# Kernel tuning notes

Measured on AMD Instinct MI355X. Metric: run time of the kernel, lower is better.

Reference implementation:

```python
import jax, jax.numpy as jnp
import numpy as np

B, D, E, N = 2048, 4096, 512, 8192
BN_EPS = 1e-5
COS_EPS = 1e-8


def setup_inputs() -> dict:
    key = jax.random.key(0)
    k1, k2, k3, k4, k5 = jax.random.split(key, 5)
    vf = jax.random.normal(k1, (B, D), dtype=jnp.float32)
    p_wfs = jax.random.normal(k2, (B, D), dtype=jnp.float32)
    n_wfs = jax.random.normal(k3, (N, E), dtype=jnp.float32)
    # BatchNorm1d(4096) affine params (default init gamma=1, beta=0; use random-ish gamma for generality)
    gamma = jnp.ones((D,), dtype=jnp.float32)
    beta = jnp.zeros((D,), dtype=jnp.float32)
    # Linear(D -> E)
    lim = 1.0 / np.sqrt(D)
    W = jax.random.uniform(k4, (E, D), dtype=jnp.float32, minval=-lim, maxval=lim)
    b = jax.random.uniform(k5, (E,), dtype=jnp.float32, minval=-lim, maxval=lim)
    return {"vf": vf, "p_wfs": p_wfs, "n_wfs": n_wfs, "gamma": gamma, "beta": beta, "W": W, "b": b}


def _row_normalize(x, eps=COS_EPS):
    nrm = jnp.sqrt(jnp.sum(x * x, axis=-1, keepdims=True))
    return x / jnp.maximum(nrm, eps)


def reference(vf, p_wfs, n_wfs, gamma, beta, W, b):
    # BatchNorm1d in training mode: batch mean / biased variance over the batch dim
    mean = jnp.mean(vf, axis=0)
    var = jnp.mean((vf - mean) ** 2, axis=0)
    vfn = (vf - mean) * (gamma / jnp.sqrt(var + BN_EPS)) + beta  # [B, D]

    # Linear + ReLU embedding
    emb = jax.nn.relu(vfn @ W.T + b)  # [B, E]

    # p_e: row-wise cosine(normed vf, p_wfs) -> [B]
    p_e = jnp.sum(_row_normalize(vfn) * _row_normalize(p_wfs), axis=-1)

    # n_e: cosine(emb[v], n_wfs[n]) for all v,n -> one normalized GEMM [B, N]
    n_e = _row_normalize(emb) @ _row_normalize(n_wfs).T

    n_neg = n_wfs.shape[0]
    n_e_stack = n_e.reshape(-1, 1)                      # [B*N, 1]
    p_e_stack = jnp.repeat(p_e, n_neg).reshape(-1, 1)   # [B*N, 1], p_e[v] repeated N times
    return (n_e_stack, p_e_stack)
```

## Files before the change

### kernel.cpp

```cpp
#include <hip/hip_runtime.h>
#include <stdint.h>
#include <stddef.h>

#define B_ 2048
#define D_ 4096
#define E_ 512
#define N_ 8192
#define SPLITK 4

typedef unsigned short ushort_t;
typedef __attribute__((ext_vector_type(8))) short short8;
typedef __attribute__((ext_vector_type(4))) float floatx4;
typedef __attribute__((ext_vector_type(4))) unsigned short ushort4_t;

__device__ __forceinline__ void async_load16(const void* g, void* l) {
  __builtin_amdgcn_global_load_lds((__attribute__((address_space(1))) void*)(g),
                                   (__attribute__((address_space(3))) void*)(l), 16, 0, 0);
}

__device__ __forceinline__ ushort_t f2bf(float f) {
  unsigned int u = __float_as_uint(f);
  unsigned int r = (u + 0x7fffu + ((u >> 16) & 1u)) >> 16;
  return (ushort_t)r;
}
__device__ __forceinline__ float bf2f(ushort_t h) {
  return __uint_as_float(((unsigned int)h) << 16);
}

__global__ __launch_bounds__(256) void bn_partial(const float* __restrict__ vf,
                                                  float* __restrict__ psum,
                                                  float* __restrict__ psq) {
  int d4 = blockIdx.x * 256 + threadIdx.x;
  int chunk = blockIdx.y;
  floatx4 s = {0.f, 0.f, 0.f, 0.f}, q = {0.f, 0.f, 0.f, 0.f};
  int r0 = chunk * 32;
  for (int r = r0; r < r0 + 32; ++r) {
    floatx4 v = ((const floatx4*)(vf + (size_t)r * D_))[d4];
    s += v; q += v * v;
  }
  ((floatx4*)(psum + (size_t)chunk * D_))[d4] = s;
  ((floatx4*)(psq  + (size_t)chunk * D_))[d4] = q;
}

__global__ __launch_bounds__(256) void prep_all(const float* __restrict__ psum,
                                                const float* __restrict__ psq,
                                                const float* __restrict__ gamma,
                                                const float* __restrict__ beta,
                                                const float* __restrict__ W,
                                                const float* __restrict__ nw,
                                                float* __restrict__ scale,
                                                float* __restrict__ shift,
                                                ushort_t* __restrict__ wb,
                                                ushort_t* __restrict__ nwb,
                                                float* __restrict__ inv_nw) {
  int bid = blockIdx.x;
  if (bid < 4) {
    int d4 = bid * 256 + threadIdx.x;
    floatx4 s = {0.f, 0.f, 0.f, 0.f}, q = {0.f, 0.f, 0.f, 0.f};
    for (int c = 0; c < 64; ++c) {
      s += ((const floatx4*)(psum + (size_t)c * D_))[d4];
      q += ((const floatx4*)(psq  + (size_t)c * D_))[d4];
    }
    floatx4 g = ((const floatx4*)gamma)[d4];
    floatx4 bt = ((const floatx4*)beta)[d4];
    floatx4 sc, sh;
#pragma unroll
    for (int j = 0; j < 4; ++j) {
      float mean = s[j] * (1.0f / B_);
      float var  = q[j] * (1.0f / B_) - mean * mean;
      float scj  = g[j] * rsqrtf(var + 1e-5f);
      sc[j] = scj;
      sh[j] = bt[j] - mean * scj;
    }
    ((floatx4*)scale)[d4] = sc;
    ((floatx4*)shift)[d4] = sh;
  } else if (bid < 2052) {
    size_t i = ((size_t)(bid - 4) * 256 + threadIdx.x) * 4;
    floatx4 x = *(const floatx4*)(W + i);
    ushort4_t o;
#pragma unroll
    for (int j = 0; j < 4; ++j) o[j] = f2bf(x[j]);
    *(ushort4_t*)(wb + i) = o;
  } else {
    int wv = threadIdx.x >> 6, l = threadIdx.x & 63;
    int n = (bid - 2052) * 4 + wv;
    const floatx4* src = (const floatx4*)(nw + (size_t)n * E_);
    ushort4_t* dst = (ushort4_t*)(nwb + (size_t)n * E_);
    float s = 0.f;
#pragma unroll
    for (int k = 0; k < 2; ++k) {
      floatx4 x = src[l + 64 * k];
      ushort4_t o;
#pragma unroll
      for (int j = 0; j < 4; ++j) { o[j] = f2bf(x[j]); s += x[j] * x[j]; }
      dst[l + 64 * k] = o;
    }
    for (int off = 32; off; off >>= 1) s += __shfl_down(s, off);
    if (l == 0) inv_nw[n] = 1.f / fmaxf(sqrtf(s), 1e-8f);
  }
}

__global__ __launch_bounds__(256) void pe_cast(const float* __restrict__ vf,
                                               const float* __restrict__ p,
                                               const float* __restrict__ scale,
                                               const float* __restrict__ shift,
                                               ushort_t* __restrict__ vfn,
                                               float* __restrict__ pe) {
  int wv = threadIdx.x >> 6, l = threadIdx.x & 63;
  int v = blockIdx.x * 4 + wv;
  const floatx4* vf4 = (const floatx4*)(vf + (size_t)v * D_);
  const floatx4* p4  = (const floatx4*)(p  + (size_t)v * D_);
  const floatx4* sc4 = (const floatx4*)scale;
  const floatx4* sh4 = (const floatx4*)shift;
  ushort_t* vrow = vfn + (size_t)v * D_;
  float sd = 0.f, sa = 0.f, sb = 0.f;
#pragma unroll 4
  for (int k = 0; k < 16; ++k) {
    int i = l + 64 * k;
    floatx4 x = vf4[i], y = p4[i], s = sc4[i], t = sh4[i];
    ushort4_t o;
#pragma unroll
    for (int j = 0; j < 4; ++j) {
      float xn = x[j] * s[j] + t[j];
      o[j] = f2bf(xn);
      sd += xn * y[j]; sa += xn * xn; sb += y[j] * y[j];
    }
    *(ushort4_t*)(vrow + i * 4) = o;
  }
  for (int off = 32; off; off >>= 1) {
    sd += __shfl_down(sd, off); sa += __shfl_down(sa, off); sb += __shfl_down(sb, off);
  }
  if (l == 0) {
    float na = fmaxf(sqrtf(sa), 1e-8f), nb = fmaxf(sqrtf(sb), 1e-8f);
    pe[v] = sd / (na * nb);
  }
}

template <int BM, int BN, int BK, int WCOLS, int MT, int NT>
__device__ __forceinline__ void gemm_core(const ushort_t* __restrict__ A,
                                          const ushort_t* __restrict__ Bt, int K,
                                          int kb, int ke, int bm0, int bn0,
                                          ushort_t* As, ushort_t* Bs,
                                          floatx4 (&acc)[MT][NT]) {
  const int tid = threadIdx.x, w = tid >> 6, l = tid & 63;
  constexpr int ISS_A = BM * BK / 2048;
  constexpr int ISS_B = BN * BK / 2048;
  const int wr = w / WCOLS, wc = w % WCOLS;
  const int m16 = l & 15, q = l >> 4;

  for (int k0 = kb; k0 < ke; k0 += BK) {
#pragma unroll
    for (int i = 0; i < ISS_A; ++i) {
      int e = i * 2048 + tid * 8;
      int row = e / BK, col = e % BK;
      async_load16(A + (size_t)(bm0 + row) * K + (k0 + col), &As[i * 2048 + w * 512]);
    }
#pragma unroll
    for (int i = 0; i < ISS_B; ++i) {
      int e = i * 2048 + tid * 8;
      int row = e / BK, col = e % BK;
      async_load16(Bt + (size_t)(bn0 + row) * K + (k0 + col), &Bs[i * 2048 + w * 512]);
    }
    __syncthreads();
#pragma unroll
    for (int kc = 0; kc < BK / 32; ++kc) {
      short8 af[MT], bf[NT];
#pragma unroll
      for (int i = 0; i < MT; ++i)
        af[i] = *(const short8*)&As[(wr * (MT * 16) + i * 16 + m16) * BK + kc * 32 + q * 8];
#pragma unroll
      for (int j = 0; j < NT; ++j)
        bf[j] = *(const short8*)&Bs[(wc * (NT * 16) + j * 16 + m16) * BK + kc * 32 + q * 8];
#pragma unroll
      for (int i = 0; i < MT; ++i)
#pragma unroll
        for (int j = 0; j < NT; ++j)
          acc[i][j] = __builtin_amdgcn_mfma_f32_16x16x32_bf16(af[i], bf[j], acc[i][j], 0, 0, 0);
    }
    __syncthreads();
  }
}

__global__ __launch_bounds__(256, 2) void gemm1_splitk(const ushort_t* __restrict__ A,
                                                       const ushort_t* __restrict__ Bt,
                                                       float* __restrict__ partial) {
  __shared__ __align__(16) ushort_t As[128 * 64];
  __shared__ __align__(16) ushort_t Bs[64 * 64];
  floatx4 acc[4][2] = {};
  int bm0 = blockIdx.y * 128, bn0 = blockIdx.x * 64, s = blockIdx.z;
  int kb = s * (D_ / SPLITK);
  gemm_core<128, 64, 64, 2, 4, 2>(A, Bt, D_, kb, kb + D_ / SPLITK, bm0, bn0, As, Bs, acc);
  int tid = threadIdx.x, w = tid >> 6, l = tid & 63, m16 = l & 15, q = l >> 4;
  int wr = w >> 1, wc = w & 1;
  float* out = partial + (size_t)s * B_ * E_;
#pragma unroll
  for (int i = 0; i < 4; ++i)
#pragma unroll
    for (int j = 0; j < 2; ++j) {
      int col = bn0 + wc * 32 + j * 16 + m16;
#pragma unroll
      for (int r = 0; r < 4; ++r) {
        int row = bm0 + wr * 64 + i * 16 + q * 4 + r;
        out[(size_t)row * E_ + col] = acc[i][j][r];
      }
    }
}

__global__ __launch_bounds__(256) void gemm1_reduce(const float* __restrict__ partial,
                                                    const float* __restrict__ bias,
                                                    ushort_t* __restrict__ emb,
                                                    float* __restrict__ inv_emb) {
  int wv = threadIdx.x >> 6, l = threadIdx.x & 63;
  int row = blockIdx.x * 4 + wv;
  float sumsq = 0.f;
#pragma unroll
  for (int k = 0; k < 2; ++k) {
    int i = l + 64 * k;
    floatx4 v = {0.f, 0.f, 0.f, 0.f};
#pragma unroll
    for (int s = 0; s < SPLITK; ++s)
      v += ((const floatx4*)(partial + (size_t)s * B_ * E_ + (size_t)row * E_))[i];
    floatx4 bb = ((const floatx4*)bias)[i];
    ushort4_t o;
#pragma unroll
    for (int j = 0; j < 4; ++j) {
      float f = fmaxf(v[j] + bb[j], 0.f);
      o[j] = f2bf(f);
      float fb = bf2f(o[j]);
      sumsq += fb * fb;
    }
    ((ushort4_t*)(emb + (size_t)row * E_))[i] = o;
  }
  for (int off = 32; off; off >>= 1) sumsq += __shfl_down(sumsq, off);
  if (l == 0) inv_emb[row] = 1.f / fmaxf(sqrtf(sumsq), 1e-8f);
}

#define BAR() asm volatile("s_barrier" ::: "memory")
#define VMW(n) asm volatile("s_waitcnt vmcnt(" #n ")" ::: "memory")

__device__ __forceinline__ void stage_A2(const ushort_t* __restrict__ A, ushort_t* Abuf,
                                         int bm0, int tk, int h, int tid) {
#pragma unroll
  for (int j = 0; j < 2; ++j) {
    int off = j * 8192 + tid * 16;
    int sl = off >> 7;
    int cb = off & 127;
    int r  = ((sl >> 6) & 1) * 128 + h * 64 + (sl & 63);
    int cg = cb ^ ((sl & 7) << 4);
    async_load16(A + (size_t)(bm0 + r) * E_ + tk * 64 + (cg >> 1),
                 Abuf + h * 8192 + j * 4096 + (tid >> 6) * 512);
  }
}

__device__ __forceinline__ void stage_B2(const ushort_t* __restrict__ Bt, ushort_t* Bbuf,
                                         int bn0, int tk, int h, int tid) {
#pragma unroll
  for (int j = 0; j < 2; ++j) {
    int off = j * 8192 + tid * 16;
    int sl = off >> 7;
    int cb = off & 127;
    int r  = ((sl >> 5) & 3) * 64 + h * 32 + (sl & 31);
    int cg = cb ^ ((sl & 7) << 4);
    async_load16(Bt + (size_t)(bn0 + r) * E_ + tk * 64 + (cg >> 1),
                 Bbuf + h * 8192 + j * 4096 + (tid >> 6) * 512);
  }
}

template <int MH, int NH>
__device__ __forceinline__ void ph_loads(const ushort_t* Ab, const ushort_t* Bb,
                                         int wr, int wc, int m16, int co0, int co1,
                                         short8 (&af)[4][2], short8 (&bfr)[2][2]) {
#pragma unroll
  for (int f = 0; f < 4; ++f) {
    const ushort_t* p = Ab + (MH * 128 + wr * 64 + f * 16 + m16) * 64;
    af[f][0] = *(const short8*)(p + co0);
    af[f][1] = *(const short8*)(p + co1);
  }
#pragma unroll
  for (int g = 0; g < 2; ++g) {
    const ushort_t* p = Bb + (NH * 128 + wc * 32 + g * 16 + m16) * 64;
    bfr[g][0] = *(const short8*)(p + co0);
    bfr[g][1] = *(const short8*)(p + co1);
  }
}

template <int MH, int NH>
__device__ __forceinline__ void ph_mma(const short8 (&af)[4][2], const short8 (&bfr)[2][2],
                                       floatx4 (&acc)[2][2][4][2]) {
  __builtin_amdgcn_s_setprio(1);
#pragma unroll
  for (int kc = 0; kc < 2; ++kc)
#pragma unroll
    for (int f = 0; f < 4; ++f)
#pragma unroll
      for (int g = 0; g < 2; ++g)
        acc[MH][NH][f][g] =
            __builtin_amdgcn_mfma_f32_16x16x32_bf16(af[f][kc], bfr[g][kc], acc[MH][NH][f][g], 0, 0, 0);
  __builtin_amdgcn_s_setprio(0);
}

__device__ __forceinline__ void out2_batch(float* __restrict__ out2, float pew,
                                           int bm0, int bn0, int b, int w, int l) {
#pragma unroll
  for (int rr = 0; rr < 4; ++rr) {
    float v = __uint_as_float(__builtin_amdgcn_readlane(__float_as_uint(pew), b * 4 + rr));
    int row = bm0 + w * 32 + b * 4 + rr;
    floatx4 vv = {v, v, v, v};
    *(floatx4*)(out2 + (size_t)row * N_ + bn0 + (l << 2)) = vv;
  }
}

#define PH(MH, NH, AB, BB, STAGE, WAIT) \
  { short8 af[4][2]; short8 bfr[2][2];                                  \
    ph_loads<MH, NH>(AB, BB, wr, wc, m16, co0, co1, af, bfr);           \
    STAGE; WAIT;                                                        \
    BAR();                                                              \
    ph_mma<MH, NH>(af, bfr, acc);                                       \
    BAR(); }

__global__ __launch_bounds__(512, 2) void gemm2_8ph(const ushort_t* __restrict__ A,
                                                    const ushort_t* __restrict__ Bt,
                                                    const float* __restrict__ inv_a,
                                                    const float* __restrict__ inv_b,
                                                    const float* __restrict__ pe,
                                                    float* __restrict__ out) {
  __shared__ __align__(16) ushort_t As_[2][16384];
  __shared__ __align__(16) ushort_t Bs_[2][16384];
  const int tid = threadIdx.x, w = tid >> 6, l = tid & 63;
  const int m16 = l & 15, q = l >> 4;
  const int wr = w >> 2, wc = w & 3;
  const int bm0 = blockIdx.y * 256, bn0 = blockIdx.x * 256;
  const int swz = (m16 & 7) << 4;
  const int co0 = ((q * 16) ^ swz) >> 1;
  const int co1 = ((64 + q * 16) ^ swz) >> 1;
  float* out2 = out + (size_t)B_ * N_;

  floatx4 acc[2][2][4][2] = {};

  float pew = pe[bm0 + w * 32 + (l & 31)];
  VMW(0);

  stage_A2(A, As_[0], bm0, 0, 0, tid);
  stage_A2(A, As_[0], bm0, 0, 1, tid);
  stage_B2(Bt, Bs_[0], bn0, 0, 0, tid);
  stage_B2(Bt, Bs_[0], bn0, 0, 1, tid);
  stage_A2(A, As_[1], bm0, 1, 0, tid);
  stage_B2(Bt, Bs_[1], bn0, 1, 0, tid);
  VMW(4);
  BAR();

#pragma unroll
  for (int i = 0; i < 4; ++i) {
    const int t1 = 2 * i + 1, t2 = 2 * i + 2, t3 = 2 * i + 3;
    const bool pre = (i < 3);
    out2_batch(out2, pew, bm0, bn0, 2 * i, w, l);
    PH(0, 0, As_[0], Bs_[0], stage_A2(A, As_[1], bm0, t1, 1, tid), ;)
    PH(0, 1, As_[0], Bs_[0], stage_B2(Bt, Bs_[1], bn0, t1, 1, tid), ;)
    PH(1, 0, As_[0], Bs_[0], if (pre) stage_A2(A, As_[0], bm0, t2, 0, tid), ;)
    PH(1, 1, As_[0], Bs_[0],
       if (pre) stage_B2(Bt, Bs_[0], bn0, t2, 0, tid),
       if (pre) { VMW(4); } else { VMW(0); })
    out2_batch(out2, pew, bm0, bn0, 2 * i + 1, w, l);
    PH(0, 0, As_[1], Bs_[1], if (pre) stage_A2(A, As_[0], bm0, t2, 1, tid), ;)
    PH(0, 1, As_[1], Bs_[1], if (pre) stage_B2(Bt, Bs_[0], bn0, t2, 1, tid), ;)
    PH(1, 0, As_[1], Bs_[1], if (pre) stage_A2(A, As_[1], bm0, t3, 0, tid), ;)
    PH(1, 1, As_[1], Bs_[1],
       if (pre) stage_B2(Bt, Bs_[1], bn0, t3, 0, tid),
       if (pre) { VMW(4); })
  }

  float ibv[2][2];
#pragma unroll
  for (int nh = 0; nh < 2; ++nh)
#pragma unroll
    for (int g = 0; g < 2; ++g)
      ibv[nh][g] = inv_b[bn0 + wc * 64 + nh * 32 + g * 16 + m16];
#pragma unroll
  for (int mh = 0; mh < 2; ++mh)
#pragma unroll
    for (int f = 0; f < 4; ++f)
#pragma unroll
      for (int rr = 0; rr < 4; ++rr) {
        int row = bm0 + wr * 128 + mh * 64 + f * 16 + q * 4 + rr;
        float ia = inv_a[row];
        size_t base = (size_t)row * N_ + bn0 + wc * 64;
#pragma unroll
        for (int nh = 0; nh < 2; ++nh)
#pragma unroll
          for (int g = 0; g < 2; ++g)
            out[base + nh * 32 + g * 16 + m16] = acc[mh][nh][f][g][rr] * ia * ibv[nh][g];
      }
}

extern "C" void kernel_launch(void* const* d_in, const int* in_sizes, int n_in,
                              void* d_out, int out_size, void* d_ws, size_t ws_size,
                              hipStream_t stream) {
  (void)in_sizes; (void)n_in; (void)out_size; (void)ws_size;
  const float* vf    = (const float*)d_in[0];
  const float* p_wfs = (const float*)d_in[1];
  const float* n_wfs = (const float*)d_in[2];
  const float* gamma = (const float*)d_in[3];
  const float* beta  = (const float*)d_in[4];
  const float* W     = (const float*)d_in[5];
  const float* bias  = (const float*)d_in[6];
  float* out = (float*)d_out;

  char* ws = (char*)d_ws;
  float* psum    = (float*)ws;  ws += (size_t)64 * D_ * 4;
  float* psq     = (float*)ws;  ws += (size_t)64 * D_ * 4;
  float* scale   = (float*)ws;  ws += (size_t)D_ * 4;
  float* shift   = (float*)ws;  ws += (size_t)D_ * 4;
  float* pe      = (float*)ws;  ws += (size_t)B_ * 4;
  float* inv_nw  = (float*)ws;  ws += (size_t)N_ * 4;
  float* inv_emb = (float*)ws;  ws += (size_t)B_ * 4;
  float* partial = (float*)ws;  ws += (size_t)SPLITK * B_ * E_ * 4;
  ushort_t* vfn  = (ushort_t*)ws;  ws += (size_t)B_ * D_ * 2;
  ushort_t* wb   = (ushort_t*)ws;  ws += (size_t)E_ * D_ * 2;
  ushort_t* nwb  = (ushort_t*)ws;  ws += (size_t)N_ * E_ * 2;
  ushort_t* emb  = (ushort_t*)ws;  ws += (size_t)B_ * E_ * 2;

  bn_partial<<<dim3(D_ / 1024, 64), 256, 0, stream>>>(vf, psum, psq);
  prep_all<<<4 + 2048 + N_ / 4, 256, 0, stream>>>(psum, psq, gamma, beta, W, n_wfs,
                                                  scale, shift, wb, nwb, inv_nw);
  pe_cast<<<B_ / 4, 256, 0, stream>>>(vf, p_wfs, scale, shift, vfn, pe);
  gemm1_splitk<<<dim3(E_ / 64, B_ / 128, SPLITK), 256, 0, stream>>>(vfn, wb, partial);
  gemm1_reduce<<<B_ / 4, 256, 0, stream>>>(partial, bias, emb, inv_emb);
  gemm2_8ph<<<dim3(N_ / 256, B_ / 256), 512, 0, stream>>>(emb, nwb, inv_emb, inv_nw, pe, out);
}
```

Before: 271.7 us.

## Double-buffer split-K GEMM1 with swizzled LDS and async prefetch pipeline

Replaces the generic single-buffered gemm_core in the first split-K GEMM with a dedicated two-stage pipeline. Global-to-LDS loads for tile t+2 are issued while MFMAs run on the current tile, with explicit vmcnt/lgkmcnt waits and raw barriers. An XOR swizzle on LDS columns is added to cut bank conflicts, along with s_setprio around the MFMA block. The cost is double the LDS per block, which may reduce occupancy, and more delicate hand-written wait and barrier ordering.

```diff
diff --git a/kernel.cpp b/kernel.cpp
--- a/kernel.cpp
+++ b/kernel.cpp
@@ -26,6 +26,10 @@
 __device__ __forceinline__ float bf2f(ushort_t h) {
   return __uint_as_float(((unsigned int)h) << 16);
 }
+
+#define BAR() asm volatile("s_barrier" ::: "memory")
+#define VMW(n) asm volatile("s_waitcnt vmcnt(" #n ")" ::: "memory")
+#define LGKM0() asm volatile("s_waitcnt lgkmcnt(0)" ::: "memory")
 
 __global__ __launch_bounds__(256) void bn_partial(const float* __restrict__ vf,
                                                   float* __restrict__ psum,
@@ -136,63 +140,80 @@
   }
 }
 
-template <int BM, int BN, int BK, int WCOLS, int MT, int NT>
-__device__ __forceinline__ void gemm_core(const ushort_t* __restrict__ A,
-                                          const ushort_t* __restrict__ Bt, int K,
-                                          int kb, int ke, int bm0, int bn0,
-                                          ushort_t* As, ushort_t* Bs,
-                                          floatx4 (&acc)[MT][NT]) {
-  const int tid = threadIdx.x, w = tid >> 6, l = tid & 63;
-  constexpr int ISS_A = BM * BK / 2048;
-  constexpr int ISS_B = BN * BK / 2048;
-  const int wr = w / WCOLS, wc = w % WCOLS;
-  const int m16 = l & 15, q = l >> 4;
-
-  for (int k0 = kb; k0 < ke; k0 += BK) {
-#pragma unroll
-    for (int i = 0; i < ISS_A; ++i) {
-      int e = i * 2048 + tid * 8;
-      int row = e / BK, col = e % BK;
-      async_load16(A + (size_t)(bm0 + row) * K + (k0 + col), &As[i * 2048 + w * 512]);
-    }
-#pragma unroll
-    for (int i = 0; i < ISS_B; ++i) {
-      int e = i * 2048 + tid * 8;
-      int row = e / BK, col = e % BK;
-      async_load16(Bt + (size_t)(bn0 + row) * K + (k0 + col), &Bs[i * 2048 + w * 512]);
-    }
-    __syncthreads();
-#pragma unroll
-    for (int kc = 0; kc < BK / 32; ++kc) {
-      short8 af[MT], bf[NT];
-#pragma unroll
-      for (int i = 0; i < MT; ++i)
-        af[i] = *(const short8*)&As[(wr * (MT * 16) + i * 16 + m16) * BK + kc * 32 + q * 8];
-#pragma unroll
-      for (int j = 0; j < NT; ++j)
-        bf[j] = *(const short8*)&Bs[(wc * (NT * 16) + j * 16 + m16) * BK + kc * 32 + q * 8];
-#pragma unroll
-      for (int i = 0; i < MT; ++i)
-#pragma unroll
-        for (int j = 0; j < NT; ++j)
-          acc[i][j] = __builtin_amdgcn_mfma_f32_16x16x32_bf16(af[i], bf[j], acc[i][j], 0, 0, 0);
-    }
-    __syncthreads();
-  }
-}
-
 __global__ __launch_bounds__(256, 2) void gemm1_splitk(const ushort_t* __restrict__ A,
                                                        const ushort_t* __restrict__ Bt,
                                                        float* __restrict__ partial) {
-  __shared__ __align__(16) ushort_t As[128 * 64];
-  __shared__ __align__(16) ushort_t Bs[64 * 64];
+  __shared__ __align__(16) ushort_t As[2][128 * 64];
+  __shared__ __align__(16) ushort_t Bs[2][64 * 64];
   floatx4 acc[4][2] = {};
-  int bm0 = blockIdx.y * 128, bn0 = blockIdx.x * 64, s = blockIdx.z;
-  int kb = s * (D_ / SPLITK);
-  gemm_core<128, 64, 64, 2, 4, 2>(A, Bt, D_, kb, kb + D_ / SPLITK, bm0, bn0, As, Bs, acc);
-  int tid = threadIdx.x, w = tid >> 6, l = tid & 63, m16 = l & 15, q = l >> 4;
-  int wr = w >> 1, wc = w & 1;
-  float* out = partial + (size_t)s * B_ * E_;
+  const int tid = threadIdx.x, w = tid >> 6, l = tid & 63;
+  const int m16 = l & 15, q = l >> 4;
+  const int wr = w >> 1, wc = w & 1;
+  const int bm0 = blockIdx.y * 128, bn0 = blockIdx.x * 64;
+  const int kb = blockIdx.z * (D_ / SPLITK);
+
+  auto stageA = [&](int t, int b) {
+#pragma unroll
+    for (int i = 0; i < 4; ++i) {
+      int lin = i * 2048 + tid * 8;
+      int row = lin >> 6, colp = lin & 63;
+      int col = colp ^ ((row & 7) << 3);
+      async_load16(A + (size_t)(bm0 + row) * D_ + kb + t * 64 + col,
+                   &As[b][i * 2048 + w * 512]);
+    }
+  };
+  auto stageB = [&](int t, int b) {
+#pragma unroll
+    for (int i = 0; i < 2; ++i) {
+      int lin = i * 2048 + tid * 8;
+      int row = lin >> 6, colp = lin & 63;
+      int col = colp ^ ((row & 7) << 3);
+      async_load16(Bt + (size_t)(bn0 + row) * D_ + kb + t * 64 + col,
+                   &Bs[b][i * 2048 + w * 512]);
+    }
+  };
+
+  stageA(0, 0); stageB(0, 0);
+  stageA(1, 1); stageB(1, 1);
+  VMW(6);
+  BAR();
+
+  for (int t = 0; t < 16; ++t) {
+    const int cur = t & 1;
+    short8 af[4][2], bf[2][2];
+#pragma unroll
+    for (int i = 0; i < 4; ++i) {
+      int arow = wr * 64 + i * 16 + m16;
+      int sw = (arow & 7) << 3;
+#pragma unroll
+      for (int kc = 0; kc < 2; ++kc)
+        af[i][kc] = *(const short8*)&As[cur][arow * 64 + ((kc * 32 + q * 8) ^ sw)];
+    }
+#pragma unroll
+    for (int j = 0; j < 2; ++j) {
+      int brow = wc * 32 + j * 16 + m16;
+      int sw = (brow & 7) << 3;
+#pragma unroll
+      for (int kc = 0; kc < 2; ++kc)
+        bf[j][kc] = *(const short8*)&Bs[cur][brow * 64 + ((kc * 32 + q * 8) ^ sw)];
+    }
+    LGKM0();
+    BAR();
+    if (t + 2 < 16) { stageA(t + 2, cur); stageB(t + 2, cur); }
+    __builtin_amdgcn_s_setprio(1);
+#pragma unroll
+    for (int kc = 0; kc < 2; ++kc)
+#pragma unroll
+      for (int i = 0; i < 4; ++i)
+#pragma unroll
+        for (int j = 0; j < 2; ++j)
+          acc[i][j] = __builtin_amdgcn_mfma_f32_16x16x32_bf16(af[i][kc], bf[j][kc], acc[i][j], 0, 0, 0);
+    __builtin_amdgcn_s_setprio(0);
+    if (t + 2 < 16) { VMW(6); } else { VMW(0); }
+    BAR();
+  }
+
+  float* out = partial + (size_t)blockIdx.z * B_ * E_;
 #pragma unroll
   for (int i = 0; i < 4; ++i)
 #pragma unroll
@@ -234,9 +255,6 @@
   for (int off = 32; off; off >>= 1) sumsq += __shfl_down(sumsq, off);
   if (l == 0) inv_emb[row] = 1.f / fmaxf(sqrtf(sumsq), 1e-8f);
 }
-
-#define BAR() asm volatile("s_barrier" ::: "memory")
-#define VMW(n) asm volatile("s_waitcnt vmcnt(" #n ")" ::: "memory")
 
 __device__ __forceinline__ void stage_A2(const ushort_t* __restrict__ A, ushort_t* Abuf,
                                          int bm0, int tk, int h, int tid) {
```

After: 267.8 us, median of 3. Within noise of the previous version (-1.4%).
